# Kernel optimization log

Measured on AMD Instinct MI355X. Metric: run time of the kernel, lower is better.

The kernel has to match this reference:

```python
import jax, jax.numpy as jnp
import numpy as np

N = 100000   # nodes
E = 1000000  # edges
F = 128      # num_features
H = 64       # hidden_size
C = 1        # num_classes
G = 128      # num graphs in batch


def gcn_conv(x, W, b, src, dst, deg_inv_sqrt):
    # PyG GCNConv: add self-loops, symmetric normalization D^-1/2 (A+I) D^-1/2, then X W + b
    h = x @ W                                   # [N, H]
    norm = deg_inv_sqrt[src] * deg_inv_sqrt[dst]  # [E]
    msg = h[src] * norm[:, None]                # gather + scale, [E, H]
    out = jnp.zeros_like(h).at[dst].add(msg)    # scatter-add to targets
    out = out + h * (deg_inv_sqrt ** 2)[:, None]  # self-loop contribution
    return out + b


def setup_inputs() -> dict:
    key = jax.random.key(0)
    ks = jax.random.split(key, 12)
    x = jax.random.normal(ks[0], (N, F), dtype=jnp.float32)
    edge_index = jax.random.randint(ks[1], (2, E), 0, N, dtype=jnp.int32).astype(jnp.int64)
    batch = jnp.sort(jax.random.randint(ks[2], (N,), 0, G, dtype=jnp.int32)).astype(jnp.int64)
    def glorot(k, fan_in, fan_out):
        s = np.float32(np.sqrt(6.0 / (fan_in + fan_out)))
        return jax.random.uniform(k, (fan_in, fan_out), jnp.float32, -s, s)
    return {
        "x": x, "edge_index": edge_index, "batch": batch,
        "W1": glorot(ks[3], F, H), "b1": jnp.zeros((H,), jnp.float32),
        "W2": glorot(ks[4], H, H), "b2": jnp.zeros((H,), jnp.float32),
        "Wl1": glorot(ks[5], H, H), "bl1": jnp.zeros((H,), jnp.float32),
        "Wl2": glorot(ks[6], H, C), "bl2": jnp.zeros((C,), jnp.float32),
    }


def reference(x, edge_index, batch, W1, b1, W2, b2, Wl1, bl1, Wl2, bl2):
    src, dst = edge_index[0], edge_index[1]
    # degree with self-loops: 1 + in-degree(target)
    deg = jnp.ones((N,), x.dtype).at[dst].add(jnp.ones((E,), x.dtype))
    deg_inv_sqrt = jax.lax.rsqrt(deg)
    h = jax.nn.relu(gcn_conv(x, W1, b1, src, dst, deg_inv_sqrt))
    h = jax.nn.relu(gcn_conv(h, W2, b2, src, dst, deg_inv_sqrt))
    g = jax.ops.segment_sum(h, batch, num_segments=G)  # global_add_pool, [G, H]
    g = jax.nn.relu(g @ Wl1 + bl1)
    out = g @ Wl2 + bl2                                # [G, 1]
    return out.squeeze(axis=1)                         # [G]
```

## Files before the change

kernel.cpp:

```cpp
#include <hip/hip_runtime.h>

#define NN 100000
#define EE 1000000
#define FF 128
#define HH 64
#define GG 128
#define NB 391
#define MMB 1563
#define GCB 2048

__device__ inline unsigned short f2bf(float f) {
    unsigned u = __float_as_uint(f);
    u += 0x7fffu + ((u >> 16) & 1u);
    return (unsigned short)(u >> 16);
}
__device__ inline float bf2f(unsigned short h) {
    return __uint_as_float((unsigned)h << 16);
}

__global__ void k_hist(const int* __restrict__ ei, int* __restrict__ cnt) {
    int e = blockIdx.x * 256 + threadIdx.x;
    if (e < EE) atomicAdd(&cnt[ei[EE + e]], 1);
}

__global__ void k_scan1(const int* __restrict__ cnt, int* __restrict__ part,
                        float* __restrict__ dis) {
    int i = blockIdx.x * 256 + threadIdx.x;
    int c = (i < NN) ? cnt[i] : 0;
    if (i < NN) dis[i] = rsqrtf((float)(c + 1));
    int v = (i < NN) ? c : 0;
    for (int o = 1; o < 64; o <<= 1) v += __shfl_xor(v, o);
    __shared__ int ws[4];
    if ((threadIdx.x & 63) == 0) ws[threadIdx.x >> 6] = v;
    __syncthreads();
    if (threadIdx.x == 0) part[blockIdx.x] = ws[0] + ws[1] + ws[2] + ws[3];
}

__global__ void k_scan2(int* __restrict__ part) {
    __shared__ int buf[512];
    int t = threadIdx.x;
    int v = (t < NB) ? part[t] : 0;
    buf[t] = v; __syncthreads();
    for (int o = 1; o < 512; o <<= 1) {
        int u = (t >= o) ? buf[t - o] : 0;
        __syncthreads();
        buf[t] += u;
        __syncthreads();
    }
    if (t < NB) part[t] = buf[t] - v;
}

__global__ void k_scan3(const int* __restrict__ cnt, const int* __restrict__ part,
                        int* __restrict__ row_ptr, int* __restrict__ cursor) {
    int i = blockIdx.x * 256 + threadIdx.x;
    int v = (i < NN) ? cnt[i] : 0;
    int lane = threadIdx.x & 63, w = threadIdx.x >> 6;
    int incl = v;
    for (int o = 1; o < 64; o <<= 1) { int u = __shfl_up(incl, o); if (lane >= o) incl += u; }
    __shared__ int ws[4];
    if (lane == 63) ws[w] = incl;
    __syncthreads();
    int woff = 0;
    for (int k = 0; k < w; ++k) woff += ws[k];
    int excl = incl - v + woff + part[blockIdx.x];
    if (i < NN) {
        row_ptr[i] = excl;
        cursor[i]  = excl;
    }
    if (i == 0) row_ptr[NN] = EE;
}

template<int K, int XBF>
__device__ __forceinline__ void
mm_body(const void* __restrict__ Xv, const float* __restrict__ W,
        const float* __restrict__ dis, unsigned* __restrict__ Y8,
        float* __restrict__ S, float* __restrict__ Wl, int bid) {
    for (int i = threadIdx.x; i < K * HH; i += 256) Wl[i] = W[i];
    __syncthreads();
    const int lane = threadIdx.x & 63;
    const int wv   = threadIdx.x >> 6;
    const int c4   = (lane & 15) * 4;
    const int rsg  = lane >> 4;
    const int r0   = bid * 64 + wv * 16 + rsg * 4;

    const char* Xb = (const char*)Xv;
    const size_t rb = (size_t)K * (XBF ? 2 : 4);
    const char* xr0; const char* xr1; const char* xr2; const char* xr3;
    {
        int a = r0, b_ = r0 + 1, c = r0 + 2, d = r0 + 3;
        if (a > NN - 1) a = NN - 1;
        if (b_ > NN - 1) b_ = NN - 1;
        if (c > NN - 1) c = NN - 1;
        if (d > NN - 1) d = NN - 1;
        xr0 = Xb + (size_t)a * rb; xr1 = Xb + (size_t)b_ * rb;
        xr2 = Xb + (size_t)c * rb; xr3 = Xb + (size_t)d * rb;
    }
    float4 acc0 = {0,0,0,0}, acc1 = {0,0,0,0}, acc2 = {0,0,0,0}, acc3 = {0,0,0,0};

#pragma unroll 8
    for (int k4 = 0; k4 < K / 4; ++k4) {
        float4 x0, x1, x2, x3;
        if (XBF) {
            ushort4 u0 = *(const ushort4*)(xr0 + k4 * 8);
            ushort4 u1 = *(const ushort4*)(xr1 + k4 * 8);
            ushort4 u2 = *(const ushort4*)(xr2 + k4 * 8);
            ushort4 u3 = *(const ushort4*)(xr3 + k4 * 8);
            x0 = {bf2f(u0.x), bf2f(u0.y), bf2f(u0.z), bf2f(u0.w)};
            x1 = {bf2f(u1.x), bf2f(u1.y), bf2f(u1.z), bf2f(u1.w)};
            x2 = {bf2f(u2.x), bf2f(u2.y), bf2f(u2.z), bf2f(u2.w)};
            x3 = {bf2f(u3.x), bf2f(u3.y), bf2f(u3.z), bf2f(u3.w)};
        } else {
            x0 = *(const float4*)(xr0 + k4 * 16);
            x1 = *(const float4*)(xr1 + k4 * 16);
            x2 = *(const float4*)(xr2 + k4 * 16);
            x3 = *(const float4*)(xr3 + k4 * 16);
        }
        const float4 w0 = *(const float4*)&Wl[(k4 * 4 + 0) * HH + c4];
        const float4 w1 = *(const float4*)&Wl[(k4 * 4 + 1) * HH + c4];
        const float4 w2 = *(const float4*)&Wl[(k4 * 4 + 2) * HH + c4];
        const float4 w3 = *(const float4*)&Wl[(k4 * 4 + 3) * HH + c4];
#define FMA4(A, XS) \
        A.x = fmaf(XS.x, w0.x, A.x); A.y = fmaf(XS.x, w0.y, A.y); \
        A.z = fmaf(XS.x, w0.z, A.z); A.w = fmaf(XS.x, w0.w, A.w); \
        A.x = fmaf(XS.y, w1.x, A.x); A.y = fmaf(XS.y, w1.y, A.y); \
        A.z = fmaf(XS.y, w1.z, A.z); A.w = fmaf(XS.y, w1.w, A.w); \
        A.x = fmaf(XS.z, w2.x, A.x); A.y = fmaf(XS.z, w2.y, A.y); \
        A.z = fmaf(XS.z, w2.z, A.z); A.w = fmaf(XS.z, w2.w, A.w); \
        A.x = fmaf(XS.w, w3.x, A.x); A.y = fmaf(XS.w, w3.y, A.y); \
        A.z = fmaf(XS.w, w3.z, A.z); A.w = fmaf(XS.w, w3.w, A.w);
        FMA4(acc0, x0) FMA4(acc1, x1) FMA4(acc2, x2) FMA4(acc3, x3)
#undef FMA4
    }
#define STORE(I, A) { \
        const int r = r0 + I; \
        if (r < NN) { \
            const float d = dis[r]; \
            const float ax = A.x * d, ay = A.y * d, az = A.z * d, aw = A.w * d; \
            float m = fmaxf(fmaxf(fabsf(ax), fabsf(ay)), fmaxf(fabsf(az), fabsf(aw))); \
            m = fmaxf(m, __shfl_xor(m, 1)); m = fmaxf(m, __shfl_xor(m, 2)); \
            m = fmaxf(m, __shfl_xor(m, 4)); m = fmaxf(m, __shfl_xor(m, 8)); \
            const float inv = 127.0f / m; \
            int q0 = __float2int_rn(ax * inv), q1 = __float2int_rn(ay * inv); \
            int q2 = __float2int_rn(az * inv), q3 = __float2int_rn(aw * inv); \
            if (m == 0.0f) { q0 = q1 = q2 = q3 = 0; } \
            const unsigned pk = (q0 & 0xff) | ((q1 & 0xff) << 8) | \
                                ((q2 & 0xff) << 16) | ((q3 & 0xff) << 24); \
            Y8[(size_t)r * 16 + (c4 >> 2)] = pk; \
            if (c4 == 0) S[r] = m * (1.0f / 127.0f); \
        } }
    STORE(0, acc0) STORE(1, acc1) STORE(2, acc2) STORE(3, acc3)
#undef STORE
}

template<int K, int XBF>
__global__ __launch_bounds__(256) void
k_matmul_b(const void* __restrict__ X, const float* __restrict__ W,
           const float* __restrict__ dis, unsigned* __restrict__ Y8,
           float* __restrict__ S) {
    __shared__ float Wl[K * HH];
    mm_body<K, XBF>(X, W, dis, Y8, S, Wl, blockIdx.x);
}

__global__ __launch_bounds__(256) void
k_mm1_place(const float* __restrict__ X, const float* __restrict__ W,
            const float* __restrict__ dis, unsigned* __restrict__ Y8,
            float* __restrict__ S, const int* __restrict__ ei,
            int* __restrict__ cursor, int* __restrict__ srcs) {
    __shared__ float Wl[FF * HH];
    if (blockIdx.x < MMB) {
        mm_body<FF, 0>(X, W, dis, Y8, S, Wl, blockIdx.x);
    } else {
        int e = (blockIdx.x - MMB) * 256 + threadIdx.x;
        if (e < EE) {
            int d = ei[EE + e];
            int p = atomicAdd(&cursor[d], 1);
            srcs[p] = ei[e];
        }
    }
}

template<bool POOL>
__global__ __launch_bounds__(256) void
k_gconv(const int* __restrict__ row_ptr, const int* __restrict__ srcs,
        const float* __restrict__ dis, const unsigned* __restrict__ H8,
        const float* __restrict__ S, const float* __restrict__ b,
        unsigned short* __restrict__ Out, const int* __restrict__ batch,
        float* __restrict__ g) {
    const int lane = threadIdx.x & 63;
    const int li   = lane & 15;
    const int qr   = lane >> 4;
    const float bl = b[lane];

    int node = __builtin_amdgcn_readfirstlane(blockIdx.x * 4 + (threadIdx.x >> 6));
    int p0 = row_ptr[node], p1 = row_ptr[node + 1];
    int idx_l = srcs[p0 + ((lane < p1 - p0) ? lane : 0)];

    while (true) {
        const int deg = p1 - p0;
        const int F   = (deg + 1 < 64) ? deg + 1 : 64;
        int nb = (F + 7) >> 3; if (nb < 2) nb = 2;

        float ac0 = 0.f, ac1 = 0.f, ac2 = 0.f, ac3 = 0.f;
        unsigned uA0, uA1, uB0, uB1;
        float fA0, fA1, fB0, fB1;
        int ia, ib;

#define ISSUE(bi, U0, U1, G0, G1) { \
        const int iA = 8 * (bi) + qr, iB = iA + 4; \
        const int sA = __shfl(idx_l, iA), sB = __shfl(idx_l, iB); \
        const int rA = (iA < deg) ? sA : node; \
        const int rB = (iB < deg) ? sB : node; \
        U0 = H8[(size_t)rA * 16 + li];  G0 = S[rA]; \
        U1 = H8[(size_t)rB * 16 + li];  G1 = S[rB]; }
#define CONS(bi, U0, U1, G0, G1) { \
        const int iA = 8 * (bi) + qr, iB = iA + 4; \
        const float s0 = (iA <= deg) ? G0 : 0.f; \
        const float s1 = (iB <= deg) ? G1 : 0.f; \
        ac0 = fmaf(s0, (float)(signed char)(U0      ), ac0); \
        ac1 = fmaf(s0, (float)(signed char)(U0 >> 8 ), ac1); \
        ac2 = fmaf(s0, (float)(signed char)(U0 >> 16), ac2); \
        ac3 = fmaf(s0, (float)(signed char)(U0 >> 24), ac3); \
        ac0 = fmaf(s1, (float)(signed char)(U1      ), ac0); \
        ac1 = fmaf(s1, (float)(signed char)(U1 >> 8 ), ac1); \
        ac2 = fmaf(s1, (float)(signed char)(U1 >> 16), ac2); \
        ac3 = fmaf(s1, (float)(signed char)(U1 >> 24), ac3); }

        ISSUE(0, uA0, uA1, fA0, fA1) ia = 0;
        ISSUE(1, uB0, uB1, fB0, fB1) ib = 1;
        for (int bi = 2; bi < nb; ++bi) {
            CONS(ia, uA0, uA1, fA0, fA1)
            uA0 = uB0; uA1 = uB1; fA0 = fB0; fA1 = fB1; ia = ib;
            ISSUE(bi, uB0, uB1, fB0, fB1) ib = bi;
        }

        const int nnode = node + GCB * 4;
        int np0 = 0, np1 = 0, nidx = 0;
        if (nnode < NN) {
            np0 = row_ptr[nnode]; np1 = row_ptr[nnode + 1];
            nidx = srcs[np0 + ((lane < np1 - np0) ? lane : 0)];
        }

        CONS(ia, uA0, uA1, fA0, fA1)
        CONS(ib, uB0, uB1, fB0, fB1)
#undef ISSUE
#undef CONS
        if (deg >= 64) {
            for (int i = 64 + qr; i <= deg; i += 4) {
                const int r = (i < deg) ? srcs[p0 + i] : node;
                const unsigned v = H8[(size_t)r * 16 + li];
                const float s = S[r];
                ac0 = fmaf(s, (float)(signed char)(v      ), ac0);
                ac1 = fmaf(s, (float)(signed char)(v >> 8 ), ac1);
                ac2 = fmaf(s, (float)(signed char)(v >> 16), ac2);
                ac3 = fmaf(s, (float)(signed char)(v >> 24), ac3);
            }
        }

        ac0 += __shfl_xor(ac0, 16); ac0 += __shfl_xor(ac0, 32);
        ac1 += __shfl_xor(ac1, 16); ac1 += __shfl_xor(ac1, 32);
        ac2 += __shfl_xor(ac2, 16); ac2 += __shfl_xor(ac2, 32);
        ac3 += __shfl_xor(ac3, 16); ac3 += __shfl_xor(ac3, 32);
        const float c0 = __shfl(ac0, lane >> 2);
        const float c1 = __shfl(ac1, lane >> 2);
        const float c2 = __shfl(ac2, lane >> 2);
        const float c3 = __shfl(ac3, lane >> 2);
        const int m = lane & 3;
        const float acc = (m == 0) ? c0 : (m == 1) ? c1 : (m == 2) ? c2 : c3;

        float v = acc * dis[node] + bl;
        v = fmaxf(v, 0.0f);
        if (POOL) {
            unsafeAtomicAdd(&g[(size_t)batch[node] * HH + lane], v);
        } else {
            Out[(size_t)node * HH + lane] = f2bf(v);
        }

        if (nnode >= NN) break;
        node = nnode; p0 = np0; p1 = np1; idx_l = nidx;
    }
}

__global__ void k_head1(const float* __restrict__ g, const float* __restrict__ W,
                        const float* __restrict__ b, float* __restrict__ g2) {
    const int idx = blockIdx.x * 256 + threadIdx.x;
    const int row = idx >> 6;
    const int col = idx & 63;
    const float* gr = g + (size_t)row * HH;
    float acc = b[col];
#pragma unroll
    for (int k = 0; k < HH; ++k) acc = fmaf(gr[k], W[k * HH + col], acc);
    g2[idx] = acc > 0.0f ? acc : 0.0f;
}

__global__ void k_head2(const float* __restrict__ g2, const float* __restrict__ W,
                        const float* __restrict__ b, float* __restrict__ out) {
    const int r = threadIdx.x;
    if (r >= GG) return;
    const float* gr = g2 + (size_t)r * HH;
    float acc = 0.0f;
#pragma unroll
    for (int k = 0; k < HH; ++k) acc = fmaf(gr[k], W[k], acc);
    out[r] = acc + b[0];
}

extern "C" void kernel_launch(void* const* d_in, const int* in_sizes, int n_in,
                              void* d_out, int out_size, void* d_ws, size_t ws_size,
                              hipStream_t stream) {
    const float* x   = (const float*)d_in[0];
    const int*   ei  = (const int*)d_in[1];
    const int*   bat = (const int*)d_in[2];
    const float* W1  = (const float*)d_in[3];
    const float* b1  = (const float*)d_in[4];
    const float* W2  = (const float*)d_in[5];
    const float* b2  = (const float*)d_in[6];
    const float* Wl1 = (const float*)d_in[7];
    const float* bl1 = (const float*)d_in[8];
    const float* Wl2 = (const float*)d_in[9];
    const float* bl2 = (const float*)d_in[10];
    float* out = (float*)d_out;

    char* w = (char*)d_ws;
    float*    dis     = (float*)(w);
    int*      cnt     = (int*)  (w + 400128);
    int*      row_ptr = (int*)  (w + 800256);
    int*      cursor  = (int*)  (w + 1200640);
    int*      part    = (int*)  (w + 1600768);
    int*      srcs    = (int*)  (w + 1602816);
    float*    S       = (float*)(w + 5602816);
    unsigned* H8      = (unsigned*)(w + 6002944);
    unsigned short* A = (unsigned short*)(w + 12402944);
    float*    g       = (float*)(w + 25202944);
    float*    g2      = g + GG * HH;

    hipMemsetAsync(cnt, 0, (size_t)NN * sizeof(int), stream);
    k_hist <<<(EE + 255) / 256, 256, 0, stream>>>(ei, cnt);
    k_scan1<<<NB, 256, 0, stream>>>(cnt, part, dis);
    k_scan2<<<1, 512, 0, stream>>>(part);
    k_scan3<<<NB, 256, 0, stream>>>(cnt, part, row_ptr, cursor);

    k_mm1_place<<<MMB + (EE + 255) / 256, 256, 0, stream>>>(x, W1, dis, H8, S, ei, cursor, srcs);
    k_gconv<false><<<GCB, 256, 0, stream>>>(row_ptr, srcs, dis, H8, S, b1, A, nullptr, nullptr);

    k_matmul_b<HH, 1><<<MMB, 256, 0, stream>>>(A, W2, dis, H8, S);
    hipMemsetAsync(g, 0, (size_t)GG * HH * sizeof(float), stream);
    k_gconv<true><<<GCB, 256, 0, stream>>>(row_ptr, srcs, dis, H8, S, b2, nullptr, bat, g);

    k_head1<<<(GG * HH) / 256, 256, 0, stream>>>(g, Wl1, bl1, g2);
    k_head2<<<1, 128, 0, stream>>>(g2, Wl2, bl2, out);
}
```

Baseline: 271.7 us.

## Fuse second-layer matmul and int8 quantization into first gconv epilogue

The first aggregation kernel now multiplies each node's post-ReLU row by W2 (held in shared memory) using wave shuffles, scales by deg^-1/2, and writes int8-quantized rows with a per-row scale. This removes the separate matmul kernel along with the bf16 intermediate write and read of N×64 activations. The cost is a 64-step shuffle-FMA loop per node inside the gather kernel, plus 16KB of shared memory per block, which may lower occupancy of the latency-bound gather.

```diff
diff --git a/kernel.cpp b/kernel.cpp
--- a/kernel.cpp
+++ b/kernel.cpp
@@ -9,11 +9,6 @@
 #define MMB 1563
 #define GCB 2048
 
-__device__ inline unsigned short f2bf(float f) {
-    unsigned u = __float_as_uint(f);
-    u += 0x7fffu + ((u >> 16) & 1u);
-    return (unsigned short)(u >> 16);
-}
 __device__ inline float bf2f(unsigned short h) {
     return __uint_as_float((unsigned)h << 16);
 }
@@ -70,9 +65,9 @@
     if (i == 0) row_ptr[NN] = EE;
 }
 
-template<int K, int XBF>
+template<int K>
 __device__ __forceinline__ void
-mm_body(const void* __restrict__ Xv, const float* __restrict__ W,
+mm_body(const float* __restrict__ X, const float* __restrict__ W,
         const float* __restrict__ dis, unsigned* __restrict__ Y8,
         float* __restrict__ S, float* __restrict__ Wl, int bid) {
     for (int i = threadIdx.x; i < K * HH; i += 256) Wl[i] = W[i];
@@ -83,38 +78,24 @@
     const int rsg  = lane >> 4;
     const int r0   = bid * 64 + wv * 16 + rsg * 4;
 
-    const char* Xb = (const char*)Xv;
-    const size_t rb = (size_t)K * (XBF ? 2 : 4);
-    const char* xr0; const char* xr1; const char* xr2; const char* xr3;
+    const float* xr0; const float* xr1; const float* xr2; const float* xr3;
     {
         int a = r0, b_ = r0 + 1, c = r0 + 2, d = r0 + 3;
         if (a > NN - 1) a = NN - 1;
         if (b_ > NN - 1) b_ = NN - 1;
         if (c > NN - 1) c = NN - 1;
         if (d > NN - 1) d = NN - 1;
-        xr0 = Xb + (size_t)a * rb; xr1 = Xb + (size_t)b_ * rb;
-        xr2 = Xb + (size_t)c * rb; xr3 = Xb + (size_t)d * rb;
+        xr0 = X + (size_t)a * K; xr1 = X + (size_t)b_ * K;
+        xr2 = X + (size_t)c * K; xr3 = X + (size_t)d * K;
     }
     float4 acc0 = {0,0,0,0}, acc1 = {0,0,0,0}, acc2 = {0,0,0,0}, acc3 = {0,0,0,0};
 
 #pragma unroll 8
     for (int k4 = 0; k4 < K / 4; ++k4) {
-        float4 x0, x1, x2, x3;
-        if (XBF) {
-            ushort4 u0 = *(const ushort4*)(xr0 + k4 * 8);
-            ushort4 u1 = *(const ushort4*)(xr1 + k4 * 8);
-            ushort4 u2 = *(const ushort4*)(xr2 + k4 * 8);
-            ushort4 u3 = *(const ushort4*)(xr3 + k4 * 8);
-            x0 = {bf2f(u0.x), bf2f(u0.y), bf2f(u0.z), bf2f(u0.w)};
-            x1 = {bf2f(u1.x), bf2f(u1.y), bf2f(u1.z), bf2f(u1.w)};
-            x2 = {bf2f(u2.x), bf2f(u2.y), bf2f(u2.z), bf2f(u2.w)};
-            x3 = {bf2f(u3.x), bf2f(u3.y), bf2f(u3.z), bf2f(u3.w)};
-        } else {
-            x0 = *(const float4*)(xr0 + k4 * 16);
-            x1 = *(const float4*)(xr1 + k4 * 16);
-            x2 = *(const float4*)(xr2 + k4 * 16);
-            x3 = *(const float4*)(xr3 + k4 * 16);
-        }
+        const float4 x0 = *(const float4*)(xr0 + k4 * 4);
+        const float4 x1 = *(const float4*)(xr1 + k4 * 4);
+        const float4 x2 = *(const float4*)(xr2 + k4 * 4);
+        const float4 x3 = *(const float4*)(xr3 + k4 * 4);
         const float4 w0 = *(const float4*)&Wl[(k4 * 4 + 0) * HH + c4];
         const float4 w1 = *(const float4*)&Wl[(k4 * 4 + 1) * HH + c4];
         const float4 w2 = *(const float4*)&Wl[(k4 * 4 + 2) * HH + c4];
@@ -152,15 +133,6 @@
 #undef STORE
 }
 
-template<int K, int XBF>
-__global__ __launch_bounds__(256) void
-k_matmul_b(const void* __restrict__ X, const float* __restrict__ W,
-           const float* __restrict__ dis, unsigned* __restrict__ Y8,
-           float* __restrict__ S) {
-    __shared__ float Wl[K * HH];
-    mm_body<K, XBF>(X, W, dis, Y8, S, Wl, blockIdx.x);
-}
-
 __global__ __launch_bounds__(256) void
 k_mm1_place(const float* __restrict__ X, const float* __restrict__ W,
             const float* __restrict__ dis, unsigned* __restrict__ Y8,
@@ -168,7 +140,7 @@
             int* __restrict__ cursor, int* __restrict__ srcs) {
     __shared__ float Wl[FF * HH];
     if (blockIdx.x < MMB) {
-        mm_body<FF, 0>(X, W, dis, Y8, S, Wl, blockIdx.x);
+        mm_body<FF>(X, W, dis, Y8, S, Wl, blockIdx.x);
     } else {
         int e = (blockIdx.x - MMB) * 256 + threadIdx.x;
         if (e < EE) {
@@ -179,13 +151,19 @@
     }
 }
 
-template<bool POOL>
+template<int MODE>
 __global__ __launch_bounds__(256) void
 k_gconv(const int* __restrict__ row_ptr, const int* __restrict__ srcs,
         const float* __restrict__ dis, const unsigned* __restrict__ H8,
         const float* __restrict__ S, const float* __restrict__ b,
-        unsigned short* __restrict__ Out, const int* __restrict__ batch,
+        const float* __restrict__ W2, unsigned* __restrict__ H8b,
+        float* __restrict__ Sb, const int* __restrict__ batch,
         float* __restrict__ g) {
+    __shared__ float W2l[HH * HH];
+    if (MODE == 1) {
+        for (int i = threadIdx.x; i < HH * HH; i += 256) W2l[i] = W2[i];
+        __syncthreads();
+    }
     const int lane = threadIdx.x & 63;
     const int li   = lane & 15;
     const int qr   = lane >> 4;
@@ -264,15 +242,35 @@
         const float c1 = __shfl(ac1, lane >> 2);
         const float c2 = __shfl(ac2, lane >> 2);
         const float c3 = __shfl(ac3, lane >> 2);
-        const int m = lane & 3;
-        const float acc = (m == 0) ? c0 : (m == 1) ? c1 : (m == 2) ? c2 : c3;
-
-        float v = acc * dis[node] + bl;
-        v = fmaxf(v, 0.0f);
-        if (POOL) {
+        const int md = lane & 3;
+        const float acc = (md == 0) ? c0 : (md == 1) ? c1 : (md == 2) ? c2 : c3;
+
+        const float dd = dis[node];
+        float v = fmaxf(acc * dd + bl, 0.0f);
+
+        if (MODE == 2) {
             unsafeAtomicAdd(&g[(size_t)batch[node] * HH + lane], v);
         } else {
-            Out[(size_t)node * HH + lane] = f2bf(v);
+            float y = 0.0f;
+#pragma unroll 8
+            for (int k = 0; k < HH; ++k)
+                y = fmaf(__shfl(v, k), W2l[k * HH + lane], y);
+            y *= dd;
+            float m = fabsf(y);
+            m = fmaxf(m, __shfl_xor(m, 1));  m = fmaxf(m, __shfl_xor(m, 2));
+            m = fmaxf(m, __shfl_xor(m, 4));  m = fmaxf(m, __shfl_xor(m, 8));
+            m = fmaxf(m, __shfl_xor(m, 16)); m = fmaxf(m, __shfl_xor(m, 32));
+            const float inv = 127.0f / m;
+            int q = __float2int_rn(y * inv);
+            if (m == 0.0f) q = 0;
+            const int base = (lane & 15) * 4;
+            const unsigned w0 = __shfl(q, base)     & 0xffu;
+            const unsigned w1 = __shfl(q, base + 1) & 0xffu;
+            const unsigned w2 = __shfl(q, base + 2) & 0xffu;
+            const unsigned w3 = __shfl(q, base + 3) & 0xffu;
+            if (lane < 16)
+                H8b[(size_t)node * 16 + lane] = w0 | (w1 << 8) | (w2 << 16) | (w3 << 24);
+            if (lane == 0) Sb[node] = m * (1.0f / 127.0f);
         }
 
         if (nnode >= NN) break;
@@ -326,10 +324,11 @@
     int*      cursor  = (int*)  (w + 1200640);
     int*      part    = (int*)  (w + 1600768);
     int*      srcs    = (int*)  (w + 1602816);
-    float*    S       = (float*)(w + 5602816);
-    unsigned* H8      = (unsigned*)(w + 6002944);
-    unsigned short* A = (unsigned short*)(w + 12402944);
-    float*    g       = (float*)(w + 25202944);
+    float*    Sa      = (float*)(w + 5602816);
+    unsigned* H8a     = (unsigned*)(w + 6002944);
+    float*    Sb      = (float*)(w + 12402944);
+    unsigned* H8b     = (unsigned*)(w + 12803072);
+    float*    g       = (float*)(w + 19203072);
     float*    g2      = g + GG * HH;
 
     hipMemsetAsync(cnt, 0, (size_t)NN * sizeof(int), stream);
@@ -338,12 +337,14 @@
     k_scan2<<<1, 512, 0, stream>>>(part);
     k_scan3<<<NB, 256, 0, stream>>>(cnt, part, row_ptr, cursor);
 
-    k_mm1_place<<<MMB + (EE + 255) / 256, 256, 0, stream>>>(x, W1, dis, H8, S, ei, cursor, srcs);
-    k_gconv<false><<<GCB, 256, 0, stream>>>(row_ptr, srcs, dis, H8, S, b1, A, nullptr, nullptr);
-
-    k_matmul_b<HH, 1><<<MMB, 256, 0, stream>>>(A, W2, dis, H8, S);
+    k_mm1_place<<<MMB + (EE + 255) / 256, 256, 0, stream>>>(x, W1, dis, H8a, Sa, ei, cursor, srcs);
     hipMemsetAsync(g, 0, (size_t)GG * HH * sizeof(float), stream);
-    k_gconv<true><<<GCB, 256, 0, stream>>>(row_ptr, srcs, dis, H8, S, b2, nullptr, bat, g);
+
+    k_gconv<1><<<GCB, 256, 0, stream>>>(row_ptr, srcs, dis, H8a, Sa, b1, W2,
+                                        H8b, Sb, nullptr, nullptr);
+
+    k_gconv<2><<<GCB, 256, 0, stream>>>(row_ptr, srcs, dis, H8b, Sb, b2, nullptr,
+                                        nullptr, nullptr, bat, g);
 
     k_head1<<<(GG * HH) / 256, 256, 0, stream>>>(g, Wl1, bl1, g2);
     k_head2<<<1, 128, 0, stream>>>(g2, Wl2, bl2, out);
```

Result: slower. 329.7 us (+21.3%).
